# Kernel tuning notes

Hardware: AMD Instinct MI355X
Metric: run time of the kernel (lower is better)

The kernel has to match this reference:

```python
import jax, jax.numpy as jnp
import numpy as np


def setup_inputs() -> dict:
    key = jax.random.key(0)
    ks = jax.random.split(key, 7)
    B, S, D, H = 8, 1024, 1024, 16
    dk = D // H
    return {
        "q": jax.random.normal(ks[0], (B, S, D), dtype=jnp.float32),
        "k": jax.random.normal(ks[1], (B, S, D), dtype=jnp.float32),
        "v": jax.random.normal(ks[2], (B, S, D), dtype=jnp.float32),
        "Wq": jax.random.normal(ks[3], (H, dk, D), dtype=jnp.float32) * 0.03,
        "Wk": jax.random.normal(ks[4], (H, dk, D), dtype=jnp.float32) * 0.03,
        "Wv": jax.random.normal(ks[5], (dk, D), dtype=jnp.float32) * 0.03,
        "Wo": jax.random.normal(ks[6], (D, dk), dtype=jnp.float32) * 0.03,
    }


def reference(q, k, v, Wq, Wk, Wv, Wo):
    # per-head projections (Linear weight layout [out, in]); shared V projection
    dk = Wq.shape[1]
    qs = jnp.einsum("bsd,hed->bhse", q, Wq)          # [B,H,S,dk]
    ks_ = jnp.einsum("btd,hed->bhte", k, Wk)         # [B,H,S,dk]
    vs = jnp.einsum("btd,ed->bte", v, Wv)            # [B,S,dk] shared across heads
    scale = jnp.sqrt(jnp.asarray(dk, dtype=qs.dtype))
    scores = jnp.einsum("bhse,bhte->bhst", qs, ks_) / scale
    attn = jax.nn.softmax(scores, axis=-1)           # [B,H,Sq,Sk]
    heads = jnp.einsum("bhst,bte->bhse", attn, vs)   # [B,H,S,dk]
    head_mean = jnp.mean(heads, axis=1)              # mean over heads -> [B,S,dk]
    outputs = jnp.einsum("bse,de->bsd", head_mean, Wo)
    attn_out = jnp.transpose(attn, (0, 2, 1, 3))     # stacked at dim=2: [B,Sq,H,Sk]
    return outputs, attn_out
```

## Files before the change

### kernel.cpp

```cpp
#include <hip/hip_runtime.h>
#include <hip/hip_bf16.h>


typedef __attribute__((ext_vector_type(4))) float f32x4;
typedef __attribute__((ext_vector_type(8))) short bf16x8;
typedef __attribute__((ext_vector_type(4))) short short4v;
typedef __attribute__((ext_vector_type(4))) unsigned int uint4v;
typedef __attribute__((ext_vector_type(2))) unsigned int uint2v;

#define MFMA16(a, b, c) __builtin_amdgcn_mfma_f32_16x16x32_bf16((a), (b), (c), 0, 0, 0)

#define GLL16(gp, lp)                                                          \
  __builtin_amdgcn_global_load_lds(                                            \
      (const __attribute__((address_space(1))) void*)(gp),                     \
      (__attribute__((address_space(3))) void*)(lp), 16, 0, 0)

__device__ __forceinline__ unsigned int rne16(float f) {
  unsigned int u = __float_as_uint(f);
  return u + 0x7fffu + ((u >> 16) & 1u);
}
__device__ __forceinline__ unsigned int pack2bf(float a, float b) {
  return (rne16(a) >> 16) | (rne16(b) & 0xffff0000u);
}
__device__ __forceinline__ short f2bf(float f) {
  return (short)(rne16(f) >> 16);
}
__device__ __forceinline__ float bf2f(short s) {
  return __uint_as_float(((unsigned int)(unsigned short)s) << 16);
}

__global__ __launch_bounds__(256) void cvt_kernel(
    const float* __restrict__ q, const float* __restrict__ k,
    const float* __restrict__ Wq, const float* __restrict__ Wk,
    short* __restrict__ qb, short* __restrict__ kb,
    short* __restrict__ Wqb, short* __restrict__ Wkb)
{
  const int y = blockIdx.y;
  const float* src = (y == 0) ? q : (y == 1) ? k : (y == 2) ? Wq : Wk;
  short* dst = (y == 0) ? qb : (y == 1) ? kb : (y == 2) ? Wqb : Wkb;
  const int n = (y < 2) ? (8 * 1024 * 1024) : (1024 * 1024);
  const int i = (blockIdx.x * 256 + threadIdx.x) * 8;
  if (i >= n) return;
  const float4 a = *(const float4*)&src[i];
  const float4 b = *(const float4*)&src[i + 4];
  uint4v o = {pack2bf(a.x, a.y), pack2bf(a.z, a.w),
              pack2bf(b.x, b.y), pack2bf(b.z, b.w)};
  *(uint4v*)&dst[i] = o;
}

__global__ __launch_bounds__(256) void proj_qk_kernel(
    const short* __restrict__ qb, const short* __restrict__ kb,
    const short* __restrict__ Wqb, const short* __restrict__ Wkb,
    __hip_bfloat16* __restrict__ qs, __hip_bfloat16* __restrict__ ks)
{
  const int K = 1024, N = 1024;
  __shared__ short a_lds[128 * 32];
  __shared__ short b_lds[128 * 32];
  const int tid = threadIdx.x;
  const int lane = tid & 63, wid = tid >> 6;
  const int g = lane >> 4, r = lane & 15;
  const bool isK = blockIdx.y >= 8;
  const short* A = isK ? kb : qb;
  const short* W = isK ? Wkb : Wqb;
  __hip_bfloat16* C = isK ? ks : qs;
  const float scale = isK ? 1.0f : 0.125f;
  const int m0 = blockIdx.x * 128;
  const int n0 = (blockIdx.y & 7) * 128;
  const int wm = (wid >> 1) * 64, wn = (wid & 1) * 64;

  const int Ra = wid * 32;
  const int srow = lane >> 2, sslot = lane & 3;
  const long aoff0 = (long)(m0 + Ra + srow) * K + sslot * 8;
  const long aoff1 = (long)(m0 + Ra + 16 + srow) * K + sslot * 8;
  const long boff0 = (long)(n0 + Ra + srow) * K + sslot * 8;
  const long boff1 = (long)(n0 + Ra + 16 + srow) * K + sslot * 8;

  f32x4 acc[4][4];
#pragma unroll
  for (int i = 0; i < 4; ++i)
#pragma unroll
    for (int j = 0; j < 4; ++j) acc[i][j] = (f32x4){0.f, 0.f, 0.f, 0.f};

  for (int k0 = 0; k0 < K; k0 += 32) {
    __syncthreads();
    GLL16(A + aoff0 + k0, &a_lds[Ra * 32]);
    GLL16(A + aoff1 + k0, &a_lds[(Ra + 16) * 32]);
    GLL16(W + boff0 + k0, &b_lds[Ra * 32]);
    GLL16(W + boff1 + k0, &b_lds[(Ra + 16) * 32]);
    __syncthreads();
    bf16x8 af[4], bf[4];
#pragma unroll
    for (int t = 0; t < 4; ++t) {
      af[t] = *(bf16x8*)&a_lds[(wm + t * 16 + r) * 32 + g * 8];
      bf[t] = *(bf16x8*)&b_lds[(wn + t * 16 + r) * 32 + g * 8];
    }
#pragma unroll
    for (int mt = 0; mt < 4; ++mt)
#pragma unroll
      for (int nt = 0; nt < 4; ++nt)
        acc[mt][nt] = MFMA16(af[mt], bf[nt], acc[mt][nt]);
  }

#pragma unroll
  for (int mt = 0; mt < 4; ++mt)
#pragma unroll
    for (int nt = 0; nt < 4; ++nt) {
      const int n = n0 + wn + nt * 16 + r;
#pragma unroll
      for (int j = 0; j < 4; ++j) {
        const int m = m0 + wm + mt * 16 + 4 * g + j;
        C[m * N + n] = __float2bfloat16(acc[mt][nt][j] * scale);
      }
    }
}

__global__ __launch_bounds__(256) void proj_v_kernel(
    const float* __restrict__ vin, const float* __restrict__ Wv,
    __hip_bfloat16* __restrict__ vsT)
{
  const int K = 1024;
  __shared__ short a_lds[128][40];
  __shared__ short b_lds[64][40];
  const int tid  = threadIdx.x;
  const int lane = tid & 63, wid = tid >> 6;
  const int g = lane >> 4, r = lane & 15;
  const int m0 = blockIdx.x * 128;
  const int wm = wid * 32;
  const int lrow = tid >> 3, lcol = (tid & 7) * 4;

  f32x4 acc[2][4];
#pragma unroll
  for (int i = 0; i < 2; ++i)
#pragma unroll
    for (int j = 0; j < 4; ++j) acc[i][j] = (f32x4){0.f, 0.f, 0.f, 0.f};

  for (int k0 = 0; k0 < K; k0 += 32) {
    float4 av[4], wv2[2];
#pragma unroll
    for (int p = 0; p < 4; ++p)
      av[p] = *(const float4*)&vin[(m0 + lrow + p * 32) * K + k0 + lcol];
#pragma unroll
    for (int p = 0; p < 2; ++p)
      wv2[p] = *(const float4*)&Wv[(lrow + p * 32) * K + k0 + lcol];
    __syncthreads();
#pragma unroll
    for (int p = 0; p < 4; ++p) {
      uint2v ua = {pack2bf(av[p].x, av[p].y), pack2bf(av[p].z, av[p].w)};
      *(uint2v*)&a_lds[lrow + p * 32][lcol] = ua;
    }
#pragma unroll
    for (int p = 0; p < 2; ++p) {
      uint2v uw = {pack2bf(wv2[p].x, wv2[p].y), pack2bf(wv2[p].z, wv2[p].w)};
      *(uint2v*)&b_lds[lrow + p * 32][lcol] = uw;
    }
    __syncthreads();
    bf16x8 af[2], bf[4];
#pragma unroll
    for (int t = 0; t < 2; ++t) af[t] = *(bf16x8*)&a_lds[wm + t * 16 + r][g * 8];
#pragma unroll
    for (int t = 0; t < 4; ++t) bf[t] = *(bf16x8*)&b_lds[t * 16 + r][g * 8];
#pragma unroll
    for (int mt = 0; mt < 2; ++mt)
#pragma unroll
      for (int nt = 0; nt < 4; ++nt)
        acc[mt][nt] = MFMA16(af[mt], bf[nt], acc[mt][nt]);
  }

#pragma unroll
  for (int mt = 0; mt < 2; ++mt)
#pragma unroll
    for (int nt = 0; nt < 4; ++nt) {
      const int e = nt * 16 + r;
#pragma unroll
      for (int j = 0; j < 4; ++j) {
        const int m = m0 + wm + mt * 16 + 4 * g + j;
        const int b = m >> 10, t = m & 1023;
        vsT[b * 65536 + e * 1024 + t] = __float2bfloat16(acc[mt][nt][j]);
      }
    }
}

__global__ __launch_bounds__(256, 4) void attn_kernel(
    const __hip_bfloat16* __restrict__ qs_, const __hip_bfloat16* __restrict__ ks_,
    const __hip_bfloat16* __restrict__ vsT_, float* __restrict__ attn_out,
    __hip_bfloat16* __restrict__ heads_)
{
  const int S = 1024, H = 16;
  const int tid = threadIdx.x, lane = tid & 63, kc = tid >> 6;
  const int g = lane >> 4, r = lane & 15;
  const int lin = ((int)blockIdx.x & 7) * 1024 + ((int)blockIdx.x >> 3);
  const int qb = lin & 63, h = (lin >> 6) & 15, b = lin >> 10;
  const int bh = b * H + h;
  const int qrow = qb * 16;

  __shared__ short p_big[4][16][260];
  __shared__ float l_lds[4][16];
  __shared__ float inv_lds[16];
  float (*heads_ov)[16][80] = (float (*)[16][80])p_big;

  const short* qsp = (const short*)qs_;
  const short* ksp = (const short*)ks_;
  const short* vsp = (const short*)vsT_;
  short* headsp = (short*)heads_;

  const int qidx = (b * S + qrow + r) * 1024 + h * 64;
  const bf16x8 qf0 = *(const bf16x8*)&qsp[qidx + g * 8];
  const bf16x8 qf1 = *(const bf16x8*)&qsp[qidx + 32 + g * 8];
  const int kbase = (b * S + kc * 256 + r) * 1024 + h * 64 + g * 8;

  unsigned int pk[32];
  float lsa0 = 0.f, lsa1 = 0.f, lsa2 = 0.f, lsa3 = 0.f;
#pragma unroll
  for (int i = 0; i < 4; ++i) {
    const int t0 = i * 64;
    bf16x8 kf[8];
#pragma unroll
    for (int u = 0; u < 4; ++u) {
      kf[2 * u]     = *(const bf16x8*)&ksp[kbase + (t0 + 16 * u) * 1024];
      kf[2 * u + 1] = *(const bf16x8*)&ksp[kbase + (t0 + 16 * u) * 1024 + 32];
    }
    float es[4];
#pragma unroll
    for (int u = 0; u < 4; ++u) {
      f32x4 s = (f32x4){0.f, 0.f, 0.f, 0.f};
      s = MFMA16(kf[2 * u], qf0, s);
      s = MFMA16(kf[2 * u + 1], qf1, s);
      const float e0 = __expf(s[0]), e1 = __expf(s[1]);
      const float e2 = __expf(s[2]), e3 = __expf(s[3]);
      pk[i * 8 + 2 * u]     = pack2bf(e0, e1);
      pk[i * 8 + 2 * u + 1] = pack2bf(e2, e3);
      es[u] = (e0 + e1) + (e2 + e3);
    }
    lsa0 += es[0]; lsa1 += es[1]; lsa2 += es[2]; lsa3 += es[3];
  }
  float ls = (lsa0 + lsa1) + (lsa2 + lsa3);
  ls += __shfl_xor(ls, 16);
  ls += __shfl_xor(ls, 32);
  if (g == 0) l_lds[kc][r] = ls;
  __syncthreads();
  {
    const float lf = (l_lds[0][r] + l_lds[1][r]) + (l_lds[2][r] + l_lds[3][r]);
    if (kc == 0 && g == 0) inv_lds[r] = 1.f / lf;
  }

#pragma unroll
  for (int j = 0; j < 8; ++j) {
    uint2v w0 = {pk[4 * j + 0], pk[4 * j + 1]};
    uint2v w1 = {pk[4 * j + 2], pk[4 * j + 3]};
    *(uint2v*)&p_big[kc][r][j * 32 + 4 * g] = w0;
    *(uint2v*)&p_big[kc][r][j * 32 + 16 + 4 * g] = w1;
  }
  __syncthreads();

  f32x4 hacc[4];
#pragma unroll
  for (int i = 0; i < 4; ++i) hacc[i] = (f32x4){0.f, 0.f, 0.f, 0.f};
  const int vbase = b * 65536 + r * 1024 + g * 8 + kc * 256;

#pragma unroll
  for (int j = 0; j < 8; ++j) {
    const int tcl = j * 32;
    bf16x8 vf[4];
#pragma unroll
    for (int nt = 0; nt < 4; ++nt)
      vf[nt] = *(const bf16x8*)&vsp[vbase + nt * 16384 + tcl];
    const bf16x8 pa = *(bf16x8*)&p_big[kc][r][tcl + g * 8];
#pragma unroll
    for (int nt = 0; nt < 4; ++nt)
      hacc[nt] = MFMA16(pa, vf[nt], hacc[nt]);
  }

  {
    const int half = lane >> 5, l32 = lane & 31;
#pragma unroll
    for (int rp = 0; rp < 8; ++rp) {
      const int row = rp * 2 + half;
      const bf16x8 pe = *(const bf16x8*)&p_big[kc][row][l32 * 8];
      const float invr = inv_lds[row];
      f32x4 o0, o1;
      o0[0] = bf2f(pe[0]) * invr; o0[1] = bf2f(pe[1]) * invr;
      o0[2] = bf2f(pe[2]) * invr; o0[3] = bf2f(pe[3]) * invr;
      o1[0] = bf2f(pe[4]) * invr; o1[1] = bf2f(pe[5]) * invr;
      o1[2] = bf2f(pe[6]) * invr; o1[3] = bf2f(pe[7]) * invr;
      const int base = ((b * S + qrow + row) * H + h) * S + kc * 256 + l32 * 8;
      __builtin_nontemporal_store(o0, (f32x4*)&attn_out[base]);
      __builtin_nontemporal_store(o1, (f32x4*)&attn_out[base + 4]);
    }
  }
  __syncthreads();

#pragma unroll
  for (int nt = 0; nt < 4; ++nt)
#pragma unroll
    for (int j = 0; j < 4; ++j)
      heads_ov[kc][4 * g + j][nt * 16 + r] = hacc[nt][j];
  __syncthreads();

  {
    const int row = tid >> 4, c4 = (tid & 15) * 4;
    const float invr = inv_lds[row];
    short4v hv;
#pragma unroll
    for (int i = 0; i < 4; ++i) {
      const float s4 = (heads_ov[0][row][c4 + i] + heads_ov[1][row][c4 + i]) +
                       (heads_ov[2][row][c4 + i] + heads_ov[3][row][c4 + i]);
      hv[i] = f2bf(s4 * invr);
    }
    *(short4v*)&headsp[(bh * S + qrow + row) * 64 + c4] = hv;
  }
}

__global__ __launch_bounds__(256) void out_kernel(
    const __hip_bfloat16* __restrict__ heads_, const float* __restrict__ Wo,
    float* __restrict__ out)
{
  __shared__ float hm[16][64];
  const int tid = threadIdx.x;
  const int m0 = blockIdx.x * 16;
  const short* headsp = (const short*)heads_;

  {
    const int row = tid >> 4, e4 = (tid & 15) * 4;
    const int m = m0 + row, b = m >> 10, s = m & 1023;
    float a0 = 0.f, a1 = 0.f, a2 = 0.f, a3 = 0.f;
    for (int hh = 0; hh < 16; ++hh) {
      const short4v hv =
          *(const short4v*)&headsp[((b * 16 + hh) * 1024 + s) * 64 + e4];
      a0 += bf2f(hv[0]); a1 += bf2f(hv[1]); a2 += bf2f(hv[2]); a3 += bf2f(hv[3]);
    }
    const float sc = 1.f / 16.f;
    hm[row][e4 + 0] = a0 * sc; hm[row][e4 + 1] = a1 * sc;
    hm[row][e4 + 2] = a2 * sc; hm[row][e4 + 3] = a3 * sc;
  }
  __syncthreads();

  for (int c = 0; c < 4; ++c) {
    const int d = c * 256 + tid;
    float4 wo4[16];
#pragma unroll
    for (int i = 0; i < 16; ++i) wo4[i] = *(const float4*)&Wo[d * 64 + i * 4];
    for (int row = 0; row < 16; ++row) {
      float a = 0.f;
#pragma unroll
      for (int i = 0; i < 16; ++i) {
        const float4 h4 = *(const float4*)&hm[row][i * 4];
        a += h4.x * wo4[i].x + h4.y * wo4[i].y + h4.z * wo4[i].z + h4.w * wo4[i].w;
      }
      out[(m0 + row) * 1024 + d] = a;
    }
  }
}

extern "C" void kernel_launch(void* const* d_in, const int* in_sizes, int n_in,
                              void* d_out, int out_size, void* d_ws, size_t ws_size,
                              hipStream_t stream) {
  const float* q  = (const float*)d_in[0];
  const float* k  = (const float*)d_in[1];
  const float* v  = (const float*)d_in[2];
  const float* Wq = (const float*)d_in[3];
  const float* Wk = (const float*)d_in[4];
  const float* Wv = (const float*)d_in[5];
  const float* Wo = (const float*)d_in[6];

  float* out0 = (float*)d_out;
  float* attn = out0 + (size_t)8 * 1024 * 1024;

  char* ws = (char*)d_ws;
  __hip_bfloat16* qs    = (__hip_bfloat16*)(ws);
  __hip_bfloat16* ksbuf = (__hip_bfloat16*)(ws + (16u << 20));
  __hip_bfloat16* vsT   = (__hip_bfloat16*)(ws + (32u << 20));
  __hip_bfloat16* heads = (__hip_bfloat16*)(ws + (33u << 20));
  short* qbuf  = (short*)(ws + (33u << 20));
  short* kbuf  = (short*)(ws + (49u << 20));
  short* Wqbuf = (short*)(ws + (65u << 20));
  short* Wkbuf = (short*)(ws + (67u << 20));

  dim3 blk(256);
  cvt_kernel<<<dim3(4096, 4), blk, 0, stream>>>(q, k, Wq, Wk,
                                                qbuf, kbuf, Wqbuf, Wkbuf);
  proj_qk_kernel<<<dim3(64, 16), blk, 0, stream>>>(qbuf, kbuf, Wqbuf, Wkbuf,
                                                   qs, ksbuf);
  proj_v_kernel<<<dim3(64), blk, 0, stream>>>(v, Wv, vsT);
  attn_kernel<<<dim3(8192), blk, 0, stream>>>(qs, ksbuf, vsT, attn, heads);
  out_kernel<<<dim3(512), blk, 0, stream>>>(heads, Wo, out0);
}
```

Measured before the change: 421.5 us.

## Use 8 waves per attention block and keep P in registers for PV and output

Each attention block now runs 512 threads, so eight waves each own 128 keys instead of four waves owning 256. Key rows are permuted so the MFMA score output already matches the A-operand layout of the PV MFMA. That lets the exp'd probabilities be reused from registers, with no LDS round-trip or extra barrier. The attention probabilities are written straight from registers with plain stores instead of nontemporal ones, and the head reduction sums eight partials. This adds a larger LDS footprint and more waves per block, and the stores lose their nontemporal hint.

```diff
diff --git a/kernel.cpp b/kernel.cpp
--- a/kernel.cpp
+++ b/kernel.cpp
@@ -22,11 +22,14 @@
 __device__ __forceinline__ unsigned int pack2bf(float a, float b) {
   return (rne16(a) >> 16) | (rne16(b) & 0xffff0000u);
 }
-__device__ __forceinline__ short f2bf(float f) {
-  return (short)(rne16(f) >> 16);
-}
 __device__ __forceinline__ float bf2f(short s) {
   return __uint_as_float(((unsigned int)(unsigned short)s) << 16);
+}
+__device__ __forceinline__ float bflo(unsigned int u) {
+  return __uint_as_float(u << 16);
+}
+__device__ __forceinline__ float bfhi(unsigned int u) {
+  return __uint_as_float(u & 0xffff0000u);
 }
 
 __global__ __launch_bounds__(256) void cvt_kernel(
@@ -180,7 +183,7 @@
     }
 }
 
-__global__ __launch_bounds__(256, 4) void attn_kernel(
+__global__ __launch_bounds__(512, 6) void attn_kernel(
     const __hip_bfloat16* __restrict__ qs_, const __hip_bfloat16* __restrict__ ks_,
     const __hip_bfloat16* __restrict__ vsT_, float* __restrict__ attn_out,
     __hip_bfloat16* __restrict__ heads_)
@@ -193,10 +196,9 @@
   const int bh = b * H + h;
   const int qrow = qb * 16;
 
-  __shared__ short p_big[4][16][260];
-  __shared__ float l_lds[4][16];
+  __shared__ float heads_lds[8][16][66];
+  __shared__ float l_lds[8][16];
   __shared__ float inv_lds[16];
-  float (*heads_ov)[16][80] = (float (*)[16][80])p_big;
 
   const short* qsp = (const short*)qs_;
   const short* ksp = (const short*)ks_;
@@ -206,107 +208,85 @@
   const int qidx = (b * S + qrow + r) * 1024 + h * 64;
   const bf16x8 qf0 = *(const bf16x8*)&qsp[qidx + g * 8];
   const bf16x8 qf1 = *(const bf16x8*)&qsp[qidx + 32 + g * 8];
-  const int kbase = (b * S + kc * 256 + r) * 1024 + h * 64 + g * 8;
-
-  unsigned int pk[32];
-  float lsa0 = 0.f, lsa1 = 0.f, lsa2 = 0.f, lsa3 = 0.f;
-#pragma unroll
-  for (int i = 0; i < 4; ++i) {
-    const int t0 = i * 64;
-    bf16x8 kf[8];
-#pragma unroll
-    for (int u = 0; u < 4; ++u) {
-      kf[2 * u]     = *(const bf16x8*)&ksp[kbase + (t0 + 16 * u) * 1024];
-      kf[2 * u + 1] = *(const bf16x8*)&ksp[kbase + (t0 + 16 * u) * 1024 + 32];
-    }
-    float es[4];
-#pragma unroll
-    for (int u = 0; u < 4; ++u) {
+
+  const int perm_r = 8 * (r >> 2) + (r & 3);
+  const int kpb = (b * S + kc * 128 + perm_r) * 1024 + h * 64 + g * 8;
+
+  unsigned int pk[16];
+  float lsa0 = 0.f, lsa1 = 0.f;
+#pragma unroll
+  for (int c = 0; c < 4; ++c) {
+#pragma unroll
+    for (int u = 0; u < 2; ++u) {
+      const int ko = (c * 32 + 4 * u) * 1024;
+      const bf16x8 klo = *(const bf16x8*)&ksp[kpb + ko];
+      const bf16x8 khi = *(const bf16x8*)&ksp[kpb + ko + 32];
       f32x4 s = (f32x4){0.f, 0.f, 0.f, 0.f};
-      s = MFMA16(kf[2 * u], qf0, s);
-      s = MFMA16(kf[2 * u + 1], qf1, s);
+      s = MFMA16(klo, qf0, s);
+      s = MFMA16(khi, qf1, s);
       const float e0 = __expf(s[0]), e1 = __expf(s[1]);
       const float e2 = __expf(s[2]), e3 = __expf(s[3]);
-      pk[i * 8 + 2 * u]     = pack2bf(e0, e1);
-      pk[i * 8 + 2 * u + 1] = pack2bf(e2, e3);
-      es[u] = (e0 + e1) + (e2 + e3);
-    }
-    lsa0 += es[0]; lsa1 += es[1]; lsa2 += es[2]; lsa3 += es[3];
-  }
-  float ls = (lsa0 + lsa1) + (lsa2 + lsa3);
+      pk[c * 4 + 2 * u]     = pack2bf(e0, e1);
+      pk[c * 4 + 2 * u + 1] = pack2bf(e2, e3);
+      if (u == 0) lsa0 += (e0 + e1) + (e2 + e3);
+      else        lsa1 += (e0 + e1) + (e2 + e3);
+    }
+  }
+  float ls = lsa0 + lsa1;
   ls += __shfl_xor(ls, 16);
   ls += __shfl_xor(ls, 32);
   if (g == 0) l_lds[kc][r] = ls;
   __syncthreads();
-  {
-    const float lf = (l_lds[0][r] + l_lds[1][r]) + (l_lds[2][r] + l_lds[3][r]);
-    if (kc == 0 && g == 0) inv_lds[r] = 1.f / lf;
-  }
-
-#pragma unroll
-  for (int j = 0; j < 8; ++j) {
-    uint2v w0 = {pk[4 * j + 0], pk[4 * j + 1]};
-    uint2v w1 = {pk[4 * j + 2], pk[4 * j + 3]};
-    *(uint2v*)&p_big[kc][r][j * 32 + 4 * g] = w0;
-    *(uint2v*)&p_big[kc][r][j * 32 + 16 + 4 * g] = w1;
-  }
-  __syncthreads();
+  const float lf = ((l_lds[0][r] + l_lds[1][r]) + (l_lds[2][r] + l_lds[3][r])) +
+                   ((l_lds[4][r] + l_lds[5][r]) + (l_lds[6][r] + l_lds[7][r]));
+  const float inv = 1.f / lf;
+  if (kc == 0 && g == 0) inv_lds[r] = inv;
 
   f32x4 hacc[4];
 #pragma unroll
   for (int i = 0; i < 4; ++i) hacc[i] = (f32x4){0.f, 0.f, 0.f, 0.f};
-  const int vbase = b * 65536 + r * 1024 + g * 8 + kc * 256;
-
-#pragma unroll
-  for (int j = 0; j < 8; ++j) {
-    const int tcl = j * 32;
+  const int vbase = b * 65536 + r * 1024 + g * 8 + kc * 128;
+  const int arow = ((b * S + qrow + r) * H + h) * S + kc * 128;
+
+#pragma unroll
+  for (int c = 0; c < 4; ++c) {
+    const int tcl = c * 32;
     bf16x8 vf[4];
 #pragma unroll
     for (int nt = 0; nt < 4; ++nt)
       vf[nt] = *(const bf16x8*)&vsp[vbase + nt * 16384 + tcl];
-    const bf16x8 pa = *(bf16x8*)&p_big[kc][r][tcl + g * 8];
+    uint4v pu = {pk[4 * c + 0], pk[4 * c + 1], pk[4 * c + 2], pk[4 * c + 3]};
+    const bf16x8 pa = __builtin_bit_cast(bf16x8, pu);
 #pragma unroll
     for (int nt = 0; nt < 4; ++nt)
       hacc[nt] = MFMA16(pa, vf[nt], hacc[nt]);
-  }
+    f32x4 o0, o1;
+    o0[0] = bflo(pk[4 * c + 0]) * inv; o0[1] = bfhi(pk[4 * c + 0]) * inv;
+    o0[2] = bflo(pk[4 * c + 1]) * inv; o0[3] = bfhi(pk[4 * c + 1]) * inv;
+    o1[0] = bflo(pk[4 * c + 2]) * inv; o1[1] = bfhi(pk[4 * c + 2]) * inv;
+    o1[2] = bflo(pk[4 * c + 3]) * inv; o1[3] = bfhi(pk[4 * c + 3]) * inv;
+    *(f32x4*)&attn_out[arow + tcl + 8 * g] = o0;
+    *(f32x4*)&attn_out[arow + tcl + 8 * g + 4] = o1;
+  }
+
+#pragma unroll
+  for (int nt = 0; nt < 4; ++nt)
+#pragma unroll
+    for (int j = 0; j < 4; ++j)
+      heads_lds[kc][4 * g + j][nt * 16 + r] = hacc[nt][j];
+  __syncthreads();
 
   {
-    const int half = lane >> 5, l32 = lane & 31;
-#pragma unroll
-    for (int rp = 0; rp < 8; ++rp) {
-      const int row = rp * 2 + half;
-      const bf16x8 pe = *(const bf16x8*)&p_big[kc][row][l32 * 8];
-      const float invr = inv_lds[row];
-      f32x4 o0, o1;
-      o0[0] = bf2f(pe[0]) * invr; o0[1] = bf2f(pe[1]) * invr;
-      o0[2] = bf2f(pe[2]) * invr; o0[3] = bf2f(pe[3]) * invr;
-      o1[0] = bf2f(pe[4]) * invr; o1[1] = bf2f(pe[5]) * invr;
-      o1[2] = bf2f(pe[6]) * invr; o1[3] = bf2f(pe[7]) * invr;
-      const int base = ((b * S + qrow + row) * H + h) * S + kc * 256 + l32 * 8;
-      __builtin_nontemporal_store(o0, (f32x4*)&attn_out[base]);
-      __builtin_nontemporal_store(o1, (f32x4*)&attn_out[base + 4]);
-    }
-  }
-  __syncthreads();
-
-#pragma unroll
-  for (int nt = 0; nt < 4; ++nt)
-#pragma unroll
-    for (int j = 0; j < 4; ++j)
-      heads_ov[kc][4 * g + j][nt * 16 + r] = hacc[nt][j];
-  __syncthreads();
-
-  {
-    const int row = tid >> 4, c4 = (tid & 15) * 4;
-    const float invr = inv_lds[row];
-    short4v hv;
-#pragma unroll
-    for (int i = 0; i < 4; ++i) {
-      const float s4 = (heads_ov[0][row][c4 + i] + heads_ov[1][row][c4 + i]) +
-                       (heads_ov[2][row][c4 + i] + heads_ov[3][row][c4 + i]);
-      hv[i] = f2bf(s4 * invr);
-    }
-    *(short4v*)&headsp[(bh * S + qrow + row) * 64 + c4] = hv;
+    const int row = tid >> 5, c2 = (tid & 31) * 2;
+    float s0 = 0.f, s1 = 0.f;
+#pragma unroll
+    for (int w = 0; w < 8; ++w) {
+      s0 += heads_lds[w][row][c2];
+      s1 += heads_lds[w][row][c2 + 1];
+    }
+    const float iv = inv_lds[row];
+    const unsigned int o = pack2bf(s0 * iv, s1 * iv);
+    *(unsigned int*)&headsp[(bh * S + qrow + row) * 64 + c2] = o;
   }
 }
 
@@ -381,6 +361,6 @@
   proj_qk_kernel<<<dim3(64, 16), blk, 0, stream>>>(qbuf, kbuf, Wqbuf, Wkbuf,
                                                    qs, ksbuf);
   proj_v_kernel<<<dim3(64), blk, 0, stream>>>(v, Wv, vsT);
-  attn_kernel<<<dim3(8192), blk, 0, stream>>>(qs, ksbuf, vsT, attn, heads);
+  attn_kernel<<<dim3(8192), dim3(512), 0, stream>>>(qs, ksbuf, vsT, attn, heads);
   out_kernel<<<dim3(512), blk, 0, stream>>>(heads, Wo, out0);
 }
```

Result: slower. 452.4 us (+7.3%).
